# Kernel tuning notes

Hardware: AMD Instinct MI355X
Metric: run time of the kernel (lower is better)

## Reference

```python
import jax, jax.numpy as jnp
import numpy as np


def setup_inputs() -> dict:
    key = jax.random.key(0)
    ks = jax.random.split(key, 12)
    N, F, S = 50000, 256, 20          # node_num, feature_dim, samp_num
    B = 8192                          # batch of target nodes
    L1, L2 = 256, 128                 # layer1_dim, layer2_dim
    D1, D2 = 256, 256                 # dec1_dim, dec2_dim
    inv = lambda d: 1.0 / np.sqrt(d)
    return {
        "features": jax.random.normal(ks[0], (N, F), jnp.float32),
        "neigh1": jax.random.randint(ks[1], (N, S), 0, N),   # sampled neighbors (layer 1)
        "neigh2": jax.random.randint(ks[2], (B, S), 0, N),   # sampled neighbors of batch nodes
        "eps": jax.random.normal(ks[3], (B, L2), jnp.float32),
        "W1": jax.random.normal(ks[4], (L1, F), jnp.float32) * inv(F),
        "W2": jax.random.normal(ks[5], (L2, L1), jnp.float32) * inv(L1),
        "W3": jax.random.normal(ks[6], (L2, L1), jnp.float32) * inv(L1),
        "Wd1": jax.random.normal(ks[7], (D1, L2), jnp.float32) * inv(L2),
        "b1": jnp.zeros((D1,), jnp.float32),
        "Wd2": jax.random.normal(ks[8], (D2, D1), jnp.float32) * inv(D1),
        "b2": jnp.zeros((D2,), jnp.float32),
        "M1": jax.random.normal(ks[9], (D2, D2), jnp.float32) * inv(D2),
        "M2": jax.random.normal(ks[10], (D2, D2), jnp.float32) * inv(D2),
    }


def reference(features, neigh1, neigh2, eps, W1, W2, W3, Wd1, b1, Wd2, b2, M1, M2):
    # --- encode: GraphSAGE mean-aggregate, gcn=True encoder (no self-concat) ---
    # layer 1: aggregate raw features over sampled neighbors for every node
    agg1 = jnp.mean(features[neigh1], axis=1)            # [N, F]
    h1 = jax.nn.relu(agg1 @ W1.T)                        # [N, L1]
    # layer 2: aggregate layer-1 embeddings over the batch nodes' sampled neighbors
    agg2 = jnp.mean(h1[neigh2], axis=1)                  # [B, L1]
    mu = jax.nn.relu(agg2 @ W2.T)                        # [B, L2]  (enc2)
    logvar = jax.nn.relu(agg2 @ W3.T)                    # [B, L2]  (enc3)
    # --- reparameterize: std = exp(logvar), h = eps*std + mu ---
    h = eps * jnp.exp(logvar) + mu                       # [B, L2]
    # --- decode ---
    o = jnp.tanh(h @ Wd1.T + b1)                         # [B, D1]
    o = o @ Wd2.T + b2                                   # [B, D2]
    emb1 = o @ M1                                        # [B, D2]
    emb2 = o @ M2                                        # [B, D2]
    # --- inner product decoder (logits, no sigmoid) ---
    adj_without_sigmoid = emb1 @ emb2.T                  # [B, B]
    return (mu, logvar, adj_without_sigmoid)
```

## Files before the change

kernel.cpp:

```cpp
#include <hip/hip_runtime.h>
#include <cstdint>
#include <cstddef>

typedef unsigned short u16;
typedef unsigned int   u32;
typedef unsigned char  u8;
typedef __attribute__((ext_vector_type(8))) short short8;
typedef __attribute__((ext_vector_type(8))) u16   u16x8;
typedef __attribute__((ext_vector_type(4))) float f32x4;
typedef __attribute__((ext_vector_type(2))) float f32x2;
typedef __attribute__((ext_vector_type(4))) u16   u16x4;

__device__ __forceinline__ float bf2f(u16 u){
  u32 x = ((u32)u) << 16; float f; __builtin_memcpy(&f, &x, 4); return f;
}
__device__ __forceinline__ u16 f2bf(float f){
  u32 x; __builtin_memcpy(&x, &f, 4);
  x += 0x7fffu + ((x >> 16) & 1u);
  return (u16)(x >> 16);
}

__device__ __forceinline__ void gload_lds16(const u16* g, u16* l){
  __builtin_amdgcn_global_load_lds((const __attribute__((address_space(1))) void*)g,
                                   (__attribute__((address_space(3))) void*)l, 16, 0, 0);
}

__global__ __launch_bounds__(256)
void fwprep(const float* __restrict__ F, const float* __restrict__ W1f,
            const float* __restrict__ M2v, const float* __restrict__ M1v,
            const float* __restrict__ W2, const float* __restrict__ W3,
            const float* __restrict__ Wd1, const float* __restrict__ Wd2,
            u8* __restrict__ FW8, u16* __restrict__ Gtb, u16* __restrict__ Wcb,
            u16* __restrict__ Wd1b, u16* __restrict__ Wd2b, int M)
{
  __shared__ u16 lds[26624];
  const int tid  = threadIdx.x;
  const int bid  = blockIdx.x;

  if (bid >= 395){
    int j = (bid - 395) * 256 + tid;
    const float* src; u16* dst;
    if (j < 8192)                 { src = W2;  dst = Wcb; }
    else if ((j -= 8192) < 8192)  { src = W3;  dst = Wcb + 32768; }
    else if ((j -= 8192) < 8192)  { src = Wd1; dst = Wd1b; }
    else { j -= 8192; src = Wd2; dst = Wd2b; }
    float4 v = ((const float4*)src)[j];
    u16x4 o; o[0]=f2bf(v.x); o[1]=f2bf(v.y); o[2]=f2bf(v.z); o[3]=f2bf(v.w);
    ((u16x4*)dst)[j] = o;
    return;
  }

  const int lane = tid & 63;
  const int wave = tid >> 6;

  if (bid >= 391){
    u16* As = lds;
    u16* Bs = lds + 8192;
    const int g = bid - 391;
    const int wm = wave >> 1, wn = wave & 1;
    const int m0 = (g >> 1) << 7, n0 = (g & 1) << 7;

    f32x4 acc[4][4];
    #pragma unroll
    for (int a = 0; a < 4; ++a)
      #pragma unroll
      for (int b = 0; b < 4; ++b)
        acc[a][b] = (f32x4){0.f, 0.f, 0.f, 0.f};

    for (int kt = 0; kt < 4; ++kt){
      const int k0 = kt * 64;
      const int f = tid * 32;
      {
        const float* sA = M2v + (size_t)(m0 + (f >> 6)) * 256 + k0 + (f & 63);
        u16 t[32];
        #pragma unroll
        for (int q = 0; q < 8; ++q){
          float4 v = *(const float4*)(sA + q * 4);
          t[q*4]=f2bf(v.x); t[q*4+1]=f2bf(v.y); t[q*4+2]=f2bf(v.z); t[q*4+3]=f2bf(v.w);
        }
        #pragma unroll
        for (int q = 0; q < 4; ++q)
          *(u16x8*)(&As[f + q*8]) = *(const u16x8*)(&t[q*8]);
      }
      {
        const float* sB = M1v + (size_t)(n0 + (f >> 6)) * 256 + k0 + (f & 63);
        u16 t[32];
        #pragma unroll
        for (int q = 0; q < 8; ++q){
          float4 v = *(const float4*)(sB + q * 4);
          t[q*4]=f2bf(v.x); t[q*4+1]=f2bf(v.y); t[q*4+2]=f2bf(v.z); t[q*4+3]=f2bf(v.w);
        }
        #pragma unroll
        for (int q = 0; q < 4; ++q)
          *(u16x8*)(&Bs[f + q*8]) = *(const u16x8*)(&t[q*8]);
      }
      __syncthreads();
      #pragma unroll
      for (int kk = 0; kk < 2; ++kk){
        const int ko = kk * 32 + (lane >> 4) * 8;
        short8 af[4], bq[4];
        #pragma unroll
        for (int mi = 0; mi < 4; ++mi)
          af[mi] = *(const short8*)(As + (wm*64 + mi*16 + (lane & 15)) * 64 + ko);
        #pragma unroll
        for (int ni = 0; ni < 4; ++ni)
          bq[ni] = *(const short8*)(Bs + (wn*64 + ni*16 + (lane & 15)) * 64 + ko);
        #pragma unroll
        for (int mi = 0; mi < 4; ++mi)
          #pragma unroll
          for (int ni = 0; ni < 4; ++ni)
            acc[mi][ni] = __builtin_amdgcn_mfma_f32_16x16x32_bf16(af[mi], bq[ni], acc[mi][ni], 0, 0, 0);
      }
      __syncthreads();
    }

    const int rbase = m0 + wm * 64 + ((lane >> 4) << 2);
    const int cbase = n0 + wn * 64 + (lane & 15);
    #pragma unroll
    for (int mi = 0; mi < 4; ++mi)
      #pragma unroll
      for (int ni = 0; ni < 4; ++ni){
        const int col = cbase + ni * 16;
        #pragma unroll
        for (int r = 0; r < 4; ++r)
          Gtb[(size_t)(rbase + mi * 16 + r) * 256 + col] = f2bf(acc[mi][ni][r]);
      }
    return;
  }

  u16* As0 = lds;         u16* As1 = lds + 5120;
  u16* Bs0 = lds + 10240; u16* Bs1 = lds + 18432;
  const int wm = wave >> 1, wn = wave & 1;
  const int m0 = bid << 7;

  f32x4 acc[4][8];
  #pragma unroll
  for (int a = 0; a < 4; ++a)
    #pragma unroll
    for (int b = 0; b < 8; ++b)
      acc[a][b] = (f32x4){0.f, 0.f, 0.f, 0.f};

  auto stage = [&](int buf, int kt){
    const int k0 = kt * 32;
    u16* Ad = buf ? As1 : As0;
    u16* Bd = buf ? Bs1 : Bs0;
    const int f = tid * 16;
    const int row = f >> 5, ku = f & 31;
    int ra = m0 + row; if (ra >= M) ra = M - 1;
    const float* sA = F + (size_t)ra * 256 + k0 + ku;
    u16 t[16];
    #pragma unroll
    for (int q = 0; q < 4; ++q){
      float4 v = *(const float4*)(sA + q * 4);
      t[q*4]=f2bf(v.x); t[q*4+1]=f2bf(v.y); t[q*4+2]=f2bf(v.z); t[q*4+3]=f2bf(v.w);
    }
    u16* dA = Ad + row * 40 + ku;
    *(u16x8*)(dA)     = *(const u16x8*)(&t[0]);
    *(u16x8*)(dA + 8) = *(const u16x8*)(&t[8]);
    const float* sB = W1f + (size_t)tid * 256 + k0;
    u16 tb[32];
    #pragma unroll
    for (int q = 0; q < 8; ++q){
      float4 v = *(const float4*)(sB + q * 4);
      tb[q*4]=f2bf(v.x); tb[q*4+1]=f2bf(v.y); tb[q*4+2]=f2bf(v.z); tb[q*4+3]=f2bf(v.w);
    }
    const int sw = (tid & 3) << 3;
    #pragma unroll
    for (int q = 0; q < 4; ++q)
      *(u16x8*)(&Bd[tid * 32 + ((q * 8) ^ sw)]) = *(const u16x8*)(&tb[q*8]);
  };

  stage(0, 0);
  __syncthreads();
  int cur = 0;
  for (int kt = 0; kt < 8; ++kt){
    if (kt + 1 < 8) stage(cur ^ 1, kt + 1);
    const u16* as = cur ? As1 : As0;
    const u16* bs = cur ? Bs1 : Bs0;
    const int ko = (lane >> 4) * 8;
    short8 af[4], bq[8];
    #pragma unroll
    for (int mi = 0; mi < 4; ++mi)
      af[mi] = *(const short8*)(as + (wm*64 + mi*16 + (lane & 15)) * 40 + ko);
    #pragma unroll
    for (int ni = 0; ni < 8; ++ni){
      const int row = wn*128 + ni*16 + (lane & 15);
      bq[ni] = *(const short8*)(bs + row * 32 + (ko ^ ((row & 3) << 3)));
    }
    #pragma unroll
    for (int mi = 0; mi < 4; ++mi)
      #pragma unroll
      for (int ni = 0; ni < 8; ++ni)
        acc[mi][ni] = __builtin_amdgcn_mfma_f32_16x16x32_bf16(af[mi], bq[ni], acc[mi][ni], 0, 0, 0);
    __syncthreads();
    cur ^= 1;
  }

  const int rbase = m0 + wm * 64 + ((lane >> 4) << 2);
  const int cbase = wn * 128 + (lane & 15);
  #pragma unroll
  for (int mi = 0; mi < 4; ++mi)
    #pragma unroll
    for (int ni = 0; ni < 8; ++ni){
      const int col = cbase + ni * 16;
      #pragma unroll
      for (int r = 0; r < 4; ++r){
        const int row = rbase + mi * 16 + r;
        if (row < M){
          const float v = acc[mi][ni][r];
          const int pk = __builtin_amdgcn_cvt_pk_fp8_f32(v, v, 0, false);
          FW8[(size_t)row * 256 + col] = (u8)(pk & 0xff);
        }
      }
    }
}

__global__ void gather_fp8(const u32* __restrict__ rows, const int* __restrict__ idx,
                           u32* __restrict__ out, int nout){
  const int pair = blockIdx.x * 4 + (threadIdx.x >> 6);
  const int lane = threadIdx.x & 63;
  const int node0 = pair * 2;
  if (node0 >= nout) return;
  const int half = lane >> 5, l31 = lane & 31;
  const int node = node0 + half;
  const int jv = (l31 < 20) ? idx[(size_t)node * 20 + l31] : 0;
  float a[8];
  #pragma unroll
  for (int k = 0; k < 8; ++k) a[k] = 0.f;
  #pragma unroll
  for (int s = 0; s < 20; ++s){
    const int j = __shfl(jv, (lane & 32) + s, 64);
    const uint2 u = *(const uint2*)(rows + (size_t)j * 64 + l31 * 2);
    f32x2 p0 = __builtin_amdgcn_cvt_pk_f32_fp8((int)u.x, false);
    f32x2 p1 = __builtin_amdgcn_cvt_pk_f32_fp8((int)u.x, true);
    f32x2 p2 = __builtin_amdgcn_cvt_pk_f32_fp8((int)u.y, false);
    f32x2 p3 = __builtin_amdgcn_cvt_pk_f32_fp8((int)u.y, true);
    a[0]+=p0[0]; a[1]+=p0[1]; a[2]+=p1[0]; a[3]+=p1[1];
    a[4]+=p2[0]; a[5]+=p2[1]; a[6]+=p3[0]; a[7]+=p3[1];
  }
  const float inv = 0.05f;
  #pragma unroll
  for (int k = 0; k < 8; ++k) a[k] = fmaxf(a[k] * inv, 0.f);
  const int w0 = __builtin_amdgcn_cvt_pk_fp8_f32(a[0], a[1], 0, false);
  const int w1 = __builtin_amdgcn_cvt_pk_fp8_f32(a[2], a[3], 0, false);
  const int w2 = __builtin_amdgcn_cvt_pk_fp8_f32(a[4], a[5], 0, false);
  const int w3 = __builtin_amdgcn_cvt_pk_fp8_f32(a[6], a[7], 0, false);
  uint2 o;
  o.x = (w0 & 0xffffu) | ((u32)(w1 & 0xffffu) << 16);
  o.y = (w2 & 0xffffu) | ((u32)(w3 & 0xffffu) << 16);
  *(uint2*)(out + (size_t)node * 64 + l31 * 2) = o;
}

__global__ __launch_bounds__(512)
void adj_gemm(const u16* __restrict__ A, const u16* __restrict__ B,
              float* __restrict__ C)
{
  __shared__ __align__(16) u16 lds[32768];
  u16* As = lds;
  u16* Bs = lds + 16384;
  const int tid  = threadIdx.x;
  const int lane = tid & 63;
  const int wave = tid >> 6;
  const int wm = wave >> 2, wn = wave & 3;
  const int bid  = blockIdx.x;
  const int xcd  = bid & 7, slot = bid >> 3;
  const int m0 = ((xcd << 2) + (slot >> 5)) << 8;
  const int n0 = (slot & 31) << 8;

  f32x4 acc[8][4];
  #pragma unroll
  for (int a = 0; a < 8; ++a)
    #pragma unroll
    for (int b = 0; b < 4; ++b)
      acc[a][b] = (f32x4){0.f, 0.f, 0.f, 0.f};

  for (int kt = 0; kt < 4; ++kt){
    const int k0 = kt * 64;
    #pragma unroll
    for (int c = 0; c < 4; ++c){
      const int f = c * 4096 + tid * 8;
      const int row = f >> 6, ksw = (f & 63) ^ ((row & 7) << 3);
      gload_lds16(A + (size_t)(m0 + row) * 256 + k0 + ksw, As + f);
    }
    #pragma unroll
    for (int c = 0; c < 4; ++c){
      const int f = c * 4096 + tid * 8;
      const int row = f >> 6, ksw = (f & 63) ^ ((row & 7) << 3);
      gload_lds16(B + (size_t)(n0 + row) * 256 + k0 + ksw, Bs + f);
    }
    __syncthreads();
    #pragma unroll
    for (int kk = 0; kk < 2; ++kk){
      const int ko = kk * 32 + (lane >> 4) * 8;
      short8 af[8], bq[4];
      #pragma unroll
      for (int mi = 0; mi < 8; ++mi){
        const int row = wm*128 + mi*16 + (lane & 15);
        af[mi] = *(const short8*)(As + row * 64 + (ko ^ ((row & 7) << 3)));
      }
      #pragma unroll
      for (int ni = 0; ni < 4; ++ni){
        const int row = wn*64 + ni*16 + (lane & 15);
        bq[ni] = *(const short8*)(Bs + row * 64 + (ko ^ ((row & 7) << 3)));
      }
      #pragma unroll
      for (int mi = 0; mi < 8; ++mi)
        #pragma unroll
        for (int ni = 0; ni < 4; ++ni)
          acc[mi][ni] = __builtin_amdgcn_mfma_f32_16x16x32_bf16(af[mi], bq[ni], acc[mi][ni], 0, 0, 0);
    }
    __syncthreads();
  }

  float* T = (float*)lds;
  #pragma unroll
  for (int c = 0; c < 8; ++c){
    if (wm == (c >> 2)){
      #pragma unroll
      for (int mi2 = 0; mi2 < 2; ++mi2){
        const int mi = (c & 3) * 2 + mi2;
        #pragma unroll
        for (int ni = 0; ni < 4; ++ni){
          const int cl = wn*64 + ni*16 + (lane & 15);
          #pragma unroll
          for (int r = 0; r < 4; ++r){
            const int lr = mi2*16 + ((lane >> 4) << 2) + r;
            T[lr * 260 + cl] = acc[mi][ni][r];
          }
        }
      }
    }
    __syncthreads();
    #pragma unroll
    for (int q = 0; q < 4; ++q){
      const int g = q * 512 + tid;
      const int r = g >> 6, col = (g & 63) * 4;
      f32x4 v = *(const f32x4*)(T + r * 260 + col);
      __builtin_nontemporal_store(v, (f32x4*)(C + (size_t)(m0 + c*32 + r) * 8192 + n0 + col));
    }
    __syncthreads();
  }
}

__global__ __launch_bounds__(256)
void decoder(const u32* __restrict__ h1, const int* __restrict__ neigh2,
             const u16* __restrict__ Wcb,
             const u16* __restrict__ Wd1b, const u16* __restrict__ Wd2b,
             const u16* __restrict__ Gtb, const float* __restrict__ eps,
             const float* __restrict__ b1, const float* __restrict__ b2,
             float* __restrict__ outMu, float* __restrict__ outLv,
             u16* __restrict__ o2g, u16* __restrict__ tmpg)
{
  __shared__ u16 lds[22528];
  u16* S  = lds;
  u16* H  = lds + 16384;
  u16* O1 = lds + 18432;
  const int tid = threadIdx.x;
  const int lane = tid & 63, wave = tid >> 6;
  const int m0 = blockIdx.x << 4;

  auto stageB = [&](const u16* G, int K, int k0){
    const int fb = wave * 4096 + lane * 8;
    #pragma unroll
    for (int c = 0; c < 8; ++c){
      int f = fb + c * 512;
      gload_lds16(G + (size_t)(f >> 6) * K + k0 + (f & 63), S + wave*4096 + c*512);
    }
  };
  auto mstep16 = [&](const u16* aC, f32x4 (&acc)[4]){
    #pragma unroll
    for (int kk = 0; kk < 2; ++kk){
      const int ko = kk * 32 + (lane >> 4) * 8;
      short8 af = *(const short8*)(aC + (lane & 15) * 64 + ko);
      #pragma unroll
      for (int ni = 0; ni < 4; ++ni){
        short8 bq = *(const short8*)(S + (wave*64 + ni*16 + (lane & 15)) * 64 + ko);
        acc[ni] = __builtin_amdgcn_mfma_f32_16x16x32_bf16(af, bq, acc[ni], 0, 0, 0);
      }
    }
  };

  {
    const int half = lane >> 5, l31 = lane & 31;
    #pragma unroll
    for (int it = 0; it < 2; ++it){
      const int lrow = it * 8 + wave * 2 + half;
      const int node = m0 + lrow;
      const int jv = (l31 < 20) ? neigh2[(size_t)node * 20 + l31] : 0;
      float a[8];
      #pragma unroll
      for (int k = 0; k < 8; ++k) a[k] = 0.f;
      #pragma unroll
      for (int s = 0; s < 20; ++s){
        const int j = __shfl(jv, (lane & 32) + s, 64);
        const uint2 u = *(const uint2*)(h1 + (size_t)j * 64 + l31 * 2);
        f32x2 p0 = __builtin_amdgcn_cvt_pk_f32_fp8((int)u.x, false);
        f32x2 p1 = __builtin_amdgcn_cvt_pk_f32_fp8((int)u.x, true);
        f32x2 p2 = __builtin_amdgcn_cvt_pk_f32_fp8((int)u.y, false);
        f32x2 p3 = __builtin_amdgcn_cvt_pk_f32_fp8((int)u.y, true);
        a[0]+=p0[0]; a[1]+=p0[1]; a[2]+=p1[0]; a[3]+=p1[1];
        a[4]+=p2[0]; a[5]+=p2[1]; a[6]+=p3[0]; a[7]+=p3[1];
      }
      const float inv = 0.05f;
      u16x8 o;
      #pragma unroll
      for (int k = 0; k < 8; ++k) o[k] = f2bf(a[k] * inv);
      const int c0 = l31 * 8;
      *(u16x8*)(O1 + (c0 >> 6) * 1024 + lrow * 64 + (c0 & 63)) = o;
    }
  }

  f32x4 accm[2], accl[2];
  #pragma unroll
  for (int b = 0; b < 2; ++b){
    accm[b] = (f32x4){0.f,0.f,0.f,0.f};
    accl[b] = (f32x4){0.f,0.f,0.f,0.f};
  }
  for (int kt = 0; kt < 4; ++kt){
    stageB(Wcb, 256, kt * 64);
    __syncthreads();
    const u16* as = O1 + kt * 1024;
    #pragma unroll
    for (int kk = 0; kk < 2; ++kk){
      const int ko = kk * 32 + (lane >> 4) * 8;
      short8 af = *(const short8*)(as + (lane & 15) * 64 + ko);
      #pragma unroll
      for (int ni = 0; ni < 2; ++ni){
        short8 bm = *(const short8*)(S + (wave*32 + ni*16 + (lane & 15)) * 64 + ko);
        short8 bl = *(const short8*)(S + (128 + wave*32 + ni*16 + (lane & 15)) * 64 + ko);
        accm[ni] = __builtin_amdgcn_mfma_f32_16x16x32_bf16(af, bm, accm[ni], 0, 0, 0);
        accl[ni] = __builtin_amdgcn_mfma_f32_16x16x32_bf16(af, bl, accl[ni], 0, 0, 0);
      }
    }
    __syncthreads();
  }
  {
    const int erow = (lane >> 4) << 2;
    #pragma unroll
    for (int ni = 0; ni < 2; ++ni){
      const int col = wave*32 + ni*16 + (lane & 15);
      #pragma unroll
      for (int r = 0; r < 4; ++r){
        const int lrow = erow + r;
        const size_t off = (size_t)(m0 + lrow) * 128 + col;
        const float m = fmaxf(accm[ni][r], 0.f);
        const float l = fmaxf(accl[ni][r], 0.f);
        __builtin_nontemporal_store(m, &outMu[off]);
        __builtin_nontemporal_store(l, &outLv[off]);
        H[(col >> 6) * 1024 + lrow * 64 + (col & 63)] = f2bf(eps[off] * expf(l) + m);
      }
    }
  }

  const int rb = (lane >> 4) << 2;
  const int cb = wave * 64 + (lane & 15);

  {
    f32x4 acc[4];
    #pragma unroll
    for (int b = 0; b < 4; ++b) acc[b] = (f32x4){0.f,0.f,0.f,0.f};
    #pragma unroll
    for (int c = 0; c < 2; ++c){
      stageB(Wd1b, 128, c * 64);
      __syncthreads();
      mstep16(H + c * 1024, acc);
      __syncthreads();
    }
    #pragma unroll
    for (int ni = 0; ni < 4; ++ni){
      const int col = cb + ni * 16;
      const float bv = b1[col];
      #pragma unroll
      for (int r = 0; r < 4; ++r)
        O1[(col >> 6) * 1024 + (rb + r) * 64 + (col & 63)] = f2bf(tanhf(acc[ni][r] + bv));
    }
    __syncthreads();
  }

  {
    f32x4 acc[4];
    #pragma unroll
    for (int b = 0; b < 4; ++b) acc[b] = (f32x4){0.f,0.f,0.f,0.f};
    for (int c = 0; c < 4; ++c){
      stageB(Wd2b, 256, c * 64);
      __syncthreads();
      mstep16(O1 + c * 1024, acc);
      __syncthreads();
    }
    #pragma unroll
    for (int ni = 0; ni < 4; ++ni){
      const int col = cb + ni * 16;
      const float bv = b2[col];
      #pragma unroll
      for (int r = 0; r < 4; ++r)
        O1[(col >> 6) * 1024 + (rb + r) * 64 + (col & 63)] = f2bf(acc[ni][r] + bv);
    }
    __syncthreads();
    #pragma unroll
    for (int q = 0; q < 2; ++q){
      const int e = q * 2048 + tid * 8;
      const int lrow = e >> 8, col = e & 255;
      *(u16x8*)(o2g + (size_t)(m0 + lrow) * 256 + col) =
        *(const u16x8*)(O1 + (col >> 6) * 1024 + lrow * 64 + (col & 63));
    }
  }

  {
    f32x4 acc[4];
    #pragma unroll
    for (int b = 0; b < 4; ++b) acc[b] = (f32x4){0.f,0.f,0.f,0.f};
    for (int c = 0; c < 4; ++c){
      stageB(Gtb, 256, c * 64);
      __syncthreads();
      mstep16(O1 + c * 1024, acc);
      __syncthreads();
    }
    #pragma unroll
    for (int ni = 0; ni < 4; ++ni){
      const int col = cb + ni * 16;
      #pragma unroll
      for (int r = 0; r < 4; ++r)
        tmpg[(size_t)(m0 + rb + r) * 256 + col] = f2bf(acc[ni][r]);
    }
  }
}

extern "C" void kernel_launch(void* const* d_in, const int* in_sizes, int n_in,
                              void* d_out, int out_size, void* d_ws, size_t ws_size,
                              hipStream_t stream){
  const float* features = (const float*)d_in[0];
  const int*   neigh1   = (const int*)  d_in[1];
  const int*   neigh2   = (const int*)  d_in[2];
  const float* eps      = (const float*)d_in[3];
  const float* W1       = (const float*)d_in[4];
  const float* W2       = (const float*)d_in[5];
  const float* W3       = (const float*)d_in[6];
  const float* Wd1      = (const float*)d_in[7];
  const float* b1       = (const float*)d_in[8];
  const float* Wd2      = (const float*)d_in[9];
  const float* b2       = (const float*)d_in[10];
  const float* M1       = (const float*)d_in[11];
  const float* M2       = (const float*)d_in[12];
  float* out = (float*)d_out;
  char*  ws  = (char*)d_ws;

  u8*  FW8  = (u8*)(ws);
  u32* h18  = (u32*)(ws + 25600000);
  u16* o2g  = (u16*)(ws + 14680064);
  u16* tmpg = (u16*)(ws + 18874368);
  u16* W1b  = (u16*)(ws + 51200000);
  u16* Wcb  = W1b  + 65536;
  u16* Wd1b = Wcb  + 65536;
  u16* Wd2b = Wd1b + 32768;
  u16* Gtb  = Wd2b + 65536;

  fwprep<<<555, 256, 0, stream>>>(features, W1, M2, M1, W2, W3, Wd1, Wd2,
                                  FW8, Gtb, Wcb, Wd1b, Wd2b, 50000);
  gather_fp8<<<6250, 256, 0, stream>>>((const u32*)FW8, neigh1, h18, 50000);
  decoder<<<512, 256, 0, stream>>>(h18, neigh2, Wcb, Wd1b, Wd2b, Gtb, eps, b1, b2,
                                   out, out + 1048576, o2g, tmpg);
  adj_gemm<<<1024, 512, 0, stream>>>(tmpg, o2g, out + 2097152);
}
```

Baseline: 171.9 us.

## Double-buffer weight tiles in decoder kernel to overlap staging with MFMA

```diff
diff --git a/kernel.cpp b/kernel.cpp
--- a/kernel.cpp
+++ b/kernel.cpp
@@ -351,30 +351,31 @@
              float* __restrict__ outMu, float* __restrict__ outLv,
              u16* __restrict__ o2g, u16* __restrict__ tmpg)
 {
-  __shared__ u16 lds[22528];
-  u16* S  = lds;
-  u16* H  = lds + 16384;
-  u16* O1 = lds + 18432;
+  __shared__ u16 lds[38912];
+  u16* S0 = lds;
+  u16* S1 = lds + 16384;
+  u16* H  = lds + 32768;
+  u16* O1 = lds + 34816;
   const int tid = threadIdx.x;
   const int lane = tid & 63, wave = tid >> 6;
   const int m0 = blockIdx.x << 4;
 
-  auto stageB = [&](const u16* G, int K, int k0){
+  auto stageB = [&](const u16* G, int K, int k0, u16* dst){
     const int fb = wave * 4096 + lane * 8;
     #pragma unroll
     for (int c = 0; c < 8; ++c){
       int f = fb + c * 512;
-      gload_lds16(G + (size_t)(f >> 6) * K + k0 + (f & 63), S + wave*4096 + c*512);
+      gload_lds16(G + (size_t)(f >> 6) * K + k0 + (f & 63), dst + wave*4096 + c*512);
     }
   };
-  auto mstep16 = [&](const u16* aC, f32x4 (&acc)[4]){
+  auto mstep16 = [&](const u16* aC, const u16* bT, f32x4 (&acc)[4]){
     #pragma unroll
     for (int kk = 0; kk < 2; ++kk){
       const int ko = kk * 32 + (lane >> 4) * 8;
       short8 af = *(const short8*)(aC + (lane & 15) * 64 + ko);
       #pragma unroll
       for (int ni = 0; ni < 4; ++ni){
-        short8 bq = *(const short8*)(S + (wave*64 + ni*16 + (lane & 15)) * 64 + ko);
+        short8 bq = *(const short8*)(bT + (wave*64 + ni*16 + (lane & 15)) * 64 + ko);
         acc[ni] = __builtin_amdgcn_mfma_f32_16x16x32_bf16(af, bq, acc[ni], 0, 0, 0);
       }
     }
@@ -416,23 +417,27 @@
     accm[b] = (f32x4){0.f,0.f,0.f,0.f};
     accl[b] = (f32x4){0.f,0.f,0.f,0.f};
   }
-  for (int kt = 0; kt < 4; ++kt){
-    stageB(Wcb, 256, kt * 64);
-    __syncthreads();
-    const u16* as = O1 + kt * 1024;
-    #pragma unroll
-    for (int kk = 0; kk < 2; ++kk){
-      const int ko = kk * 32 + (lane >> 4) * 8;
-      short8 af = *(const short8*)(as + (lane & 15) * 64 + ko);
-      #pragma unroll
-      for (int ni = 0; ni < 2; ++ni){
-        short8 bm = *(const short8*)(S + (wave*32 + ni*16 + (lane & 15)) * 64 + ko);
-        short8 bl = *(const short8*)(S + (128 + wave*32 + ni*16 + (lane & 15)) * 64 + ko);
-        accm[ni] = __builtin_amdgcn_mfma_f32_16x16x32_bf16(af, bm, accm[ni], 0, 0, 0);
-        accl[ni] = __builtin_amdgcn_mfma_f32_16x16x32_bf16(af, bl, accl[ni], 0, 0, 0);
-      }
-    }
-    __syncthreads();
+  {
+    stageB(Wcb, 256, 0, S0);
+    __syncthreads();
+    for (int kt = 0; kt < 4; ++kt){
+      if (kt < 3) stageB(Wcb, 256, (kt+1)*64, ((kt+1)&1) ? S1 : S0);
+      const u16* as = O1 + kt * 1024;
+      const u16* bs = (kt & 1) ? S1 : S0;
+      #pragma unroll
+      for (int kk = 0; kk < 2; ++kk){
+        const int ko = kk * 32 + (lane >> 4) * 8;
+        short8 af = *(const short8*)(as + (lane & 15) * 64 + ko);
+        #pragma unroll
+        for (int ni = 0; ni < 2; ++ni){
+          short8 bm = *(const short8*)(bs + (wave*32 + ni*16 + (lane & 15)) * 64 + ko);
+          short8 bl = *(const short8*)(bs + (128 + wave*32 + ni*16 + (lane & 15)) * 64 + ko);
+          accm[ni] = __builtin_amdgcn_mfma_f32_16x16x32_bf16(af, bm, accm[ni], 0, 0, 0);
+          accl[ni] = __builtin_amdgcn_mfma_f32_16x16x32_bf16(af, bl, accl[ni], 0, 0, 0);
+        }
+      }
+      __syncthreads();
+    }
   }
   {
     const int erow = (lane >> 4) << 2;
@@ -451,6 +456,9 @@
       }
     }
   }
+  stageB(Wd1b, 128, 0, S0);
+  stageB(Wd1b, 128, 64, S1);
+  __syncthreads();
 
   const int rb = (lane >> 4) << 2;
   const int cb = wave * 64 + (lane & 15);
@@ -459,21 +467,20 @@
     f32x4 acc[4];
     #pragma unroll
     for (int b = 0; b < 4; ++b) acc[b] = (f32x4){0.f,0.f,0.f,0.f};
-    #pragma unroll
-    for (int c = 0; c < 2; ++c){
-      stageB(Wd1b, 128, c * 64);
-      __syncthreads();
-      mstep16(H + c * 1024, acc);
-      __syncthreads();
-    }
+    mstep16(H, S0, acc);
+    mstep16(H + 1024, S1, acc);
+    __syncthreads();
     #pragma unroll
     for (int ni = 0; ni < 4; ++ni){
       const int col = cb + ni * 16;
       const float bv = b1[col];
       #pragma unroll
-      for (int r = 0; r < 4; ++r)
-        O1[(col >> 6) * 1024 + (rb + r) * 64 + (col & 63)] = f2bf(tanhf(acc[ni][r] + bv));
-    }
+      for (int r = 0; r < 4; ++r){
+        const int lrow = rb + r;
+        O1[(col >> 6) * 1024 + lrow * 64 + (col & 63)] = f2bf(tanhf(acc[ni][r] + bv));
+      }
+    }
+    stageB(Wd2b, 256, 0, S0);
     __syncthreads();
   }
 
@@ -482,9 +489,8 @@
     #pragma unroll
     for (int b = 0; b < 4; ++b) acc[b] = (f32x4){0.f,0.f,0.f,0.f};
     for (int c = 0; c < 4; ++c){
-      stageB(Wd2b, 256, c * 64);
-      __syncthreads();
-      mstep16(O1 + c * 1024, acc);
+      if (c < 3) stageB(Wd2b, 256, (c+1)*64, ((c+1)&1) ? S1 : S0);
+      mstep16(O1 + c*1024, (c&1) ? S1 : S0, acc);
       __syncthreads();
     }
     #pragma unroll
@@ -492,10 +498,13 @@
       const int col = cb + ni * 16;
       const float bv = b2[col];
       #pragma unroll
-      for (int r = 0; r < 4; ++r)
-        O1[(col >> 6) * 1024 + (rb + r) * 64 + (col & 63)] = f2bf(acc[ni][r] + bv);
-    }
-    __syncthreads();
+      for (int r = 0; r < 4; ++r){
+        const int lrow = rb + r;
+        O1[(col >> 6) * 1024 + lrow * 64 + (col & 63)] = f2bf(acc[ni][r] + bv);
+      }
+    }
+    __syncthreads();
+    stageB(Gtb, 256, 0, S0);
     #pragma unroll
     for (int q = 0; q < 2; ++q){
       const int e = q * 2048 + tid * 8;
@@ -503,6 +512,7 @@
       *(u16x8*)(o2g + (size_t)(m0 + lrow) * 256 + col) =
         *(const u16x8*)(O1 + (col >> 6) * 1024 + lrow * 64 + (col & 63));
     }
+    __syncthreads();
   }
 
   {
@@ -510,17 +520,18 @@
     #pragma unroll
     for (int b = 0; b < 4; ++b) acc[b] = (f32x4){0.f,0.f,0.f,0.f};
     for (int c = 0; c < 4; ++c){
-      stageB(Gtb, 256, c * 64);
-      __syncthreads();
-      mstep16(O1 + c * 1024, acc);
+      if (c < 3) stageB(Gtb, 256, (c+1)*64, ((c+1)&1) ? S1 : S0);
+      mstep16(O1 + c*1024, (c&1) ? S1 : S0, acc);
       __syncthreads();
     }
     #pragma unroll
     for (int ni = 0; ni < 4; ++ni){
       const int col = cb + ni * 16;
       #pragma unroll
-      for (int r = 0; r < 4; ++r)
-        tmpg[(size_t)(m0 + rb + r) * 256 + col] = f2bf(acc[ni][r]);
+      for (int r = 0; r < 4; ++r){
+        const int lrow = rb + r;
+        tmpg[(size_t)(m0 + lrow) * 256 + col] = f2bf(acc[ni][r]);
+      }
     }
   }
 }
```

New measurement: 170.0 us. About the same (-1.1%).
